# Kernel tuning notes

Hardware: AMD Instinct MI355X
Metric: run time of the kernel (lower is better)

Reference implementation:

```python
import jax, jax.numpy as jnp
import numpy as np

N_NODES = 50000
N_EDGES = 250000
D = 300
ATOM_VOCAB = 5001   # len(atom_map) + 1
WORD_VOCAB = 30000
N_GRAPHS = 1000
NUM_HOPS = 4


def setup_inputs() -> dict:
    key = jax.random.key(0)
    ks = jax.random.split(key, 6)
    x = jax.random.randint(ks[0], (N_NODES, 2), 0, 5000)            # (atom_id, word_id) per node
    edge_index = jax.random.randint(ks[1], (2, N_EDGES), 0, N_NODES)
    batch = jnp.sort(jax.random.randint(ks[2], (N_NODES,), 0, N_GRAPHS))
    atom_table = jax.random.normal(ks[3], (ATOM_VOCAB, D), dtype=jnp.float32) * 0.02
    word_table = jax.random.normal(ks[4], (WORD_VOCAB, D), dtype=jnp.float32) * 0.02
    W = jax.random.normal(ks[5], (D, D), dtype=jnp.float32) / jnp.sqrt(jnp.float32(D))
    b = jnp.zeros((D,), dtype=jnp.float32)
    return {"x": x, "edge_index": edge_index, "batch": batch, "num_hops": NUM_HOPS,
            "atom_table": atom_table, "word_table": word_table, "W": W, "b": b}


def reference(x, edge_index, batch, num_hops, atom_table, word_table, W, b):
    N = x.shape[0]
    # node embedding: atom + word lookup
    h = atom_table[x[:, 0]] + word_table[x[:, 1]]                    # [N, D]

    # GCN normalization with self-loops (PyG GCNConv defaults)
    loops = jnp.arange(N)
    src = jnp.concatenate([edge_index[0], loops])                    # [E+N]
    dst = jnp.concatenate([edge_index[1], loops])                    # [E+N]
    deg = jax.ops.segment_sum(jnp.ones_like(src, dtype=h.dtype), dst, num_segments=N)
    dinv = jax.lax.rsqrt(jnp.where(deg > 0, deg, 1.0))
    norm = dinv[src] * dinv[dst]                                     # [E+N]

    for _ in range(num_hops):
        hl = h @ W                                                   # [N, D] linear transform
        msg = hl[src] * norm[:, None]                                # gather + normalize
        h = jax.ops.segment_sum(msg, dst, num_segments=N) + b        # scatter-add + bias

    # global mean pool over graphs
    sums = jax.ops.segment_sum(h, batch, num_segments=N_GRAPHS)      # [G, D]
    counts = jax.ops.segment_sum(jnp.ones((N,), h.dtype), batch, num_segments=N_GRAPHS)
    return sums / jnp.clip(counts, 1.0)[:, None]
```

## Files before the change

### kernel.cpp

```cpp
#include <hip/hip_runtime.h>
#include <hip/hip_fp16.h>

#define D    300
#define DC   75
#define SCB  1024

typedef _Float16 half4v __attribute__((ext_vector_type(4)));

__global__ __launch_bounds__(256) void embed_f16(const int* __restrict__ x,
                                                 const float4* __restrict__ atomT,
                                                 const float4* __restrict__ wordT,
                                                 half4v* __restrict__ h, int N) {
    int idx = blockIdx.x * blockDim.x + threadIdx.x;
    if (idx >= N * DC) return;
    int n = idx / DC, c = idx - n * DC;
    int a = x[n * 2 + 0];
    int w = x[n * 2 + 1];
    float4 va = atomT[(size_t)a * DC + c];
    float4 vw = wordT[(size_t)w * DC + c];
    half4v o;
    o[0] = (_Float16)(va.x + vw.x);
    o[1] = (_Float16)(va.y + vw.y);
    o[2] = (_Float16)(va.z + vw.z);
    o[3] = (_Float16)(va.w + vw.w);
    h[idx] = o;
}

__global__ __launch_bounds__(256) void cnt_kernel(const int* __restrict__ dst, int* __restrict__ cnt, int E) {
    int i = blockIdx.x * blockDim.x + threadIdx.x;
    if (i < E) atomicAdd(&cnt[dst[i]], 1);
}

__global__ __launch_bounds__(SCB) void scan1_kernel(const int* __restrict__ cnt,
                                                    int* __restrict__ off, int* __restrict__ bsum,
                                                    float* __restrict__ dinv, int N) {
    __shared__ int warp_sums[16];
    const int tid = threadIdx.x;
    const int lane = tid & 63;
    const int wid = tid >> 6;
    int i = blockIdx.x * SCB + tid;
    int v = (i < N) ? cnt[i] : 0;
    if (i < N) dinv[i] = rsqrtf((float)(v + 1));
    int s = v;
    #pragma unroll
    for (int d = 1; d < 64; d <<= 1) {
        int t = __shfl_up(s, d, 64);
        if (lane >= d) s += t;
    }
    if (lane == 63) warp_sums[wid] = s;
    __syncthreads();
    if (wid == 0) {
        int ws = (lane < 16) ? warp_sums[lane] : 0;
        #pragma unroll
        for (int d = 1; d < 16; d <<= 1) {
            int t = __shfl_up(ws, d, 64);
            if (lane >= d) ws += t;
        }
        if (lane < 16) warp_sums[lane] = ws;
    }
    __syncthreads();
    int excl = (wid ? warp_sums[wid - 1] : 0) + s - v;
    if (i < N) off[i] = excl;
    if (tid == SCB - 1) bsum[blockIdx.x] = warp_sums[15];
}
__global__ __launch_bounds__(SCB) void scan2_kernel(int* __restrict__ bsum, int* __restrict__ bbase,
                                                    int* __restrict__ off, int nb, int N, int E) {
    __shared__ int warp_sums[16];
    const int tid = threadIdx.x;
    const int lane = tid & 63;
    const int wid = tid >> 6;
    int v = (tid < nb) ? bsum[tid] : 0;
    int s = v;
    #pragma unroll
    for (int d = 1; d < 64; d <<= 1) {
        int t = __shfl_up(s, d, 64);
        if (lane >= d) s += t;
    }
    if (lane == 63) warp_sums[wid] = s;
    __syncthreads();
    if (wid == 0) {
        int ws = (lane < 16) ? warp_sums[lane] : 0;
        #pragma unroll
        for (int d = 1; d < 16; d <<= 1) {
            int t = __shfl_up(ws, d, 64);
            if (lane >= d) ws += t;
        }
        if (lane < 16) warp_sums[lane] = ws;
    }
    __syncthreads();
    if (tid < nb) bbase[tid] = (wid ? warp_sums[wid - 1] : 0) + s - v;
    if (tid == 0) off[N] = E;
}
__global__ __launch_bounds__(256) void scan3_kernel(int* __restrict__ off, const int* __restrict__ bbase,
                                                    int* __restrict__ cursor, int N) {
    int i = blockIdx.x * blockDim.x + threadIdx.x;
    if (i >= N) return;
    int o = off[i] + bbase[i >> 10];
    off[i] = o;
    cursor[i] = o;
}

__global__ __launch_bounds__(256) void fill_kernel(const int* __restrict__ src, const int* __restrict__ dst,
                                                   const float* __restrict__ dinv, int* __restrict__ cursor,
                                                   int* __restrict__ csr_src, float* __restrict__ csr_w, int E) {
    int e = blockIdx.x * blockDim.x + threadIdx.x;
    if (e >= E) return;
    int s = src[e], d = dst[e];
    int slot = atomicAdd(&cursor[d], 1);
    csr_src[slot] = s;
    csr_w[slot] = dinv[s] * dinv[d];
}
__global__ __launch_bounds__(256) void seg_start_kernel(const int* __restrict__ batch,
                                                        int* __restrict__ start, int N, int G) {
    int i = blockIdx.x * blockDim.x + threadIdx.x;
    if (i >= N) return;
    int b = batch[i];
    int prev = (i == 0) ? -1 : batch[i - 1];
    for (int g = prev + 1; g <= b; ++g) start[g] = i;
    if (i == N - 1)
        for (int g = b + 1; g <= G; ++g) start[g] = N;
}

__global__ __launch_bounds__(256) void wprep1(const float* __restrict__ W, const float* __restrict__ bias,
                                              float* __restrict__ W2, float* __restrict__ w1b) {
    int bid = blockIdx.x;
    if (bid < 352) {
        int id = bid * 256 + threadIdx.x;
        if (id >= D * D) return;
        int i = id / D, j = id % D;
        float acc = 0.f;
        #pragma unroll 4
        for (int k = 0; k < D; ++k) acc = fmaf(W[i * D + k], W[k * D + j], acc);
        W2[id] = acc;
    } else {
        int j = threadIdx.x;
        if (j >= D) return;
        float acc = 0.f;
        #pragma unroll 4
        for (int k = 0; k < D; ++k) acc = fmaf(bias[k], W[k * D + j], acc);
        w1b[j] = acc;
    }
}
__global__ __launch_bounds__(256) void wprep2(const float* __restrict__ W2, const float* __restrict__ W,
                                              const float* __restrict__ w1b,
                                              float* __restrict__ W4, float* __restrict__ w2b,
                                              float* __restrict__ w3b) {
    int bid = blockIdx.x;
    if (bid < 352) {
        int id = bid * 256 + threadIdx.x;
        if (id >= D * D) return;
        int i = id / D, j = id % D;
        float acc = 0.f;
        #pragma unroll 4
        for (int k = 0; k < D; ++k) acc = fmaf(W2[i * D + k], W2[k * D + j], acc);
        W4[id] = acc;
    } else if (bid == 352) {
        int j = threadIdx.x;
        if (j >= D) return;
        float acc = 0.f;
        #pragma unroll 4
        for (int k = 0; k < D; ++k) acc = fmaf(w1b[k], W[k * D + j], acc);
        w2b[j] = acc;
    } else {
        int j = threadIdx.x;
        if (j >= D) return;
        float acc = 0.f;
        #pragma unroll 4
        for (int k = 0; k < D; ++k) acc = fmaf(w1b[k], W2[k * D + j], acc);
        w3b[j] = acc;
    }
}

__global__ __launch_bounds__(256) void gather_f16(const half4v* __restrict__ in,
                                                  const int* __restrict__ off,
                                                  const int* __restrict__ csr_src,
                                                  const float* __restrict__ csr_w,
                                                  const float* __restrict__ dinv,
                                                  const float* __restrict__ uin,
                                                  float* __restrict__ uout,
                                                  half4v* __restrict__ out, int N) {
    int idx = blockIdx.x * blockDim.x + threadIdx.x;
    if (idx >= N * DC) return;
    int n = idx / DC, c = idx - n * DC;
    float s = dinv[n]; s = s * s;
    half4v v0 = in[idx];
    float4 acc = make_float4(s * (float)v0[0], s * (float)v0[1], s * (float)v0[2], s * (float)v0[3]);
    const bool dou = (uout != nullptr) && (c == 0);
    float uacc = 0.f;
    if (dou) uacc = s * (uin ? uin[n] : 1.0f);
    int j0 = off[n], j1 = off[n + 1];
    for (int j = j0; j < j1; ++j) {
        int sn = csr_src[j];
        float w = csr_w[j];
        half4v u = in[(size_t)sn * DC + c];
        acc.x += w * (float)u[0]; acc.y += w * (float)u[1];
        acc.z += w * (float)u[2]; acc.w += w * (float)u[3];
        if (dou) uacc += w * (uin ? uin[sn] : 1.0f);
    }
    half4v o;
    o[0] = (_Float16)acc.x; o[1] = (_Float16)acc.y;
    o[2] = (_Float16)acc.z; o[3] = (_Float16)acc.w;
    out[idx] = o;
    if (dou) uout[n] = uacc;
}

__global__ __launch_bounds__(256) void pool_seg(const half4v* __restrict__ g4,
                                                const float* __restrict__ u1,
                                                const float* __restrict__ u2,
                                                const float* __restrict__ u3,
                                                const int* __restrict__ start,
                                                float* __restrict__ pg4, float* __restrict__ pu, int G) {
    int g = blockIdx.x;
    if (g >= G) return;
    int j0 = start[g], j1 = start[g + 1];
    float inv = (j1 > j0) ? 1.0f / (float)(j1 - j0) : 0.0f;
    int tid = threadIdx.x;
    if (tid < DC) {
        float4 acc = make_float4(0.f, 0.f, 0.f, 0.f);
        for (int n = j0; n < j1; ++n) {
            half4v v = g4[(size_t)n * DC + tid];
            acc.x += (float)v[0]; acc.y += (float)v[1];
            acc.z += (float)v[2]; acc.w += (float)v[3];
        }
        float4 o = make_float4(acc.x * inv, acc.y * inv, acc.z * inv, acc.w * inv);
        *(float4*)&pg4[(size_t)g * D + tid * 4] = o;
    } else if (tid == DC || tid == DC + 1 || tid == DC + 2) {
        const float* u = (tid == DC) ? u1 : (tid == DC + 1) ? u2 : u3;
        float acc = 0.f;
        for (int n = j0; n < j1; ++n) acc += u[n];
        pu[g * 4 + (tid - DC)] = acc * inv;
    } else if (tid == DC + 3) {
        pu[g * 4 + 3] = (j1 > j0) ? 1.0f : 0.0f;
    }
}

__global__ __launch_bounds__(256) void final_small(const float* __restrict__ pg4,
                                                   const float* __restrict__ pu,
                                                   const float* __restrict__ W4,
                                                   const float* __restrict__ w1b,
                                                   const float* __restrict__ w2b,
                                                   const float* __restrict__ w3b,
                                                   const float* __restrict__ bias,
                                                   float* __restrict__ out, int G) {
    __shared__ float row[D];
    int g = blockIdx.x;
    if (g >= G) return;
    int tid = threadIdx.x;
    for (int c = tid; c < D; c += 256) row[c] = pg4[(size_t)g * D + c];
    __syncthreads();
    float p1 = pu[g * 4 + 0], p2 = pu[g * 4 + 1], p3 = pu[g * 4 + 2], fl = pu[g * 4 + 3];
    for (int j = tid; j < D; j += 256) {
        float acc = 0.f;
        #pragma unroll 4
        for (int k = 0; k < D; ++k) acc = fmaf(row[k], W4[(size_t)k * D + j], acc);
        out[(size_t)g * D + j] = acc + p1 * w1b[j] + p2 * w2b[j] + p3 * w3b[j] + fl * bias[j];
    }
}

extern "C" void kernel_launch(void* const* d_in, const int* in_sizes, int n_in,
                              void* d_out, int out_size, void* d_ws, size_t ws_size,
                              hipStream_t stream) {
    (void)n_in; (void)ws_size;
    const int*   x     = (const int*)d_in[0];
    const int*   ei    = (const int*)d_in[1];
    const int*   batch = (const int*)d_in[2];
    const float* atomT = (const float*)d_in[4];
    const float* wordT = (const float*)d_in[5];
    const float* W     = (const float*)d_in[6];
    const float* bias  = (const float*)d_in[7];

    const int N = in_sizes[0] / 2;
    const int E = in_sizes[1] / 2;
    const int G = out_size / D;

    const int* src = ei;
    const int* dst = ei + E;

    _Float16* fA16   = (_Float16*)d_ws;
    _Float16* fB16   = fA16 + (size_t)N * D;
    float*    dinv   = (float*)(fB16 + (size_t)N * D);
    float*    csr_w  = dinv + N;
    float*    W2     = csr_w + E;
    float*    W4     = W2 + D * D;
    float*    w1b    = W4 + D * D;
    float*    w2b    = w1b + D;
    float*    w3b    = w2b + D;
    float*    u1     = w3b + D;
    float*    u2     = u1 + N;
    float*    u3     = u2 + N;
    float*    pg4    = u3 + N;
    float*    pu     = pg4 + (size_t)G * D;
    int*      cnt    = (int*)(pu + 4 * G);
    int*      off    = cnt + N;
    int*      cursor = off + N + 1;
    int*      csr_src= cursor + N;
    int*      bsum   = csr_src + E;
    int*      bbase  = bsum + 1024;
    int*      start  = bbase + 1024;

    const int B = 256;
    const int ndBlocks = (N * DC + B - 1) / B;
    const int nBlocks  = (N + B - 1) / B;
    const int nbScan   = (N + SCB - 1) / SCB;

    embed_f16<<<ndBlocks, B, 0, stream>>>(x, (const float4*)atomT, (const float4*)wordT, (half4v*)fA16, N);

    hipMemsetAsync(cnt, 0, (size_t)N * sizeof(int), stream);
    cnt_kernel<<<(E + B - 1) / B, B, 0, stream>>>(dst, cnt, E);
    scan1_kernel<<<nbScan, SCB, 0, stream>>>(cnt, off, bsum, dinv, N);
    scan2_kernel<<<1, SCB, 0, stream>>>(bsum, bbase, off, nbScan, N, E);
    scan3_kernel<<<nBlocks, B, 0, stream>>>(off, bbase, cursor, N);
    fill_kernel<<<(E + B - 1) / B, B, 0, stream>>>(src, dst, dinv, cursor, csr_src, csr_w, E);
    seg_start_kernel<<<nBlocks, B, 0, stream>>>(batch, start, N, G);

    wprep1<<<353, B, 0, stream>>>(W, bias, W2, w1b);
    wprep2<<<354, B, 0, stream>>>(W2, W, w1b, W4, w2b, w3b);

    gather_f16<<<ndBlocks, B, 0, stream>>>((const half4v*)fA16, off, csr_src, csr_w, dinv,
                                           nullptr, u1, (half4v*)fB16, N);
    gather_f16<<<ndBlocks, B, 0, stream>>>((const half4v*)fB16, off, csr_src, csr_w, dinv,
                                           u1, u2, (half4v*)fA16, N);
    gather_f16<<<ndBlocks, B, 0, stream>>>((const half4v*)fA16, off, csr_src, csr_w, dinv,
                                           u2, u3, (half4v*)fB16, N);
    gather_f16<<<ndBlocks, B, 0, stream>>>((const half4v*)fB16, off, csr_src, csr_w, dinv,
                                           nullptr, nullptr, (half4v*)fA16, N);

    pool_seg<<<G, B, 0, stream>>>((const half4v*)fA16, u1, u2, u3, start, pg4, pu, G);
    final_small<<<G, B, 0, stream>>>(pg4, pu, W4, w1b, w2b, w3b, bias, (float*)d_out, G);
}
```

Before: 384.2 us.

## Split node features into column panels for cache-local gathers with nontemporal CSR loads

Feature rows are now stored as 8 column panels of 10 half4 chunks each, padded from 75 to 80, and blocks are interleaved across panels. Each gather then touches a panel of about 4 MB instead of the full 30 MB feature matrix, so random neighbour reads are more likely to hit in L2/MALL. CSR index, weight loads and the output stores also use nontemporal hints so they do not evict feature data. The cost is padding waste of about 7%, CSR metadata being re-read once per panel, and changed indexing in the embed and pool kernels.

Result: slower. 574.2 us (+49.4%).

```diff
diff --git a/kernel.cpp b/kernel.cpp
--- a/kernel.cpp
+++ b/kernel.cpp
@@ -3,34 +3,40 @@
 
 #define D    300
 #define DC   75
+#define PNL  8
+#define PCH  10
 #define SCB  1024
 
 typedef _Float16 half4v __attribute__((ext_vector_type(4)));
 
-__global__ __launch_bounds__(256) void embed_f16(const int* __restrict__ x,
-                                                 const float4* __restrict__ atomT,
-                                                 const float4* __restrict__ wordT,
-                                                 half4v* __restrict__ h, int N) {
-    int idx = blockIdx.x * blockDim.x + threadIdx.x;
-    if (idx >= N * DC) return;
-    int n = idx / DC, c = idx - n * DC;
-    int a = x[n * 2 + 0];
-    int w = x[n * 2 + 1];
-    float4 va = atomT[(size_t)a * DC + c];
-    float4 vw = wordT[(size_t)w * DC + c];
-    half4v o;
-    o[0] = (_Float16)(va.x + vw.x);
-    o[1] = (_Float16)(va.y + vw.y);
-    o[2] = (_Float16)(va.z + vw.z);
-    o[3] = (_Float16)(va.w + vw.w);
-    h[idx] = o;
+__global__ __launch_bounds__(256) void embed_panel(const int* __restrict__ x,
+                                                   const float4* __restrict__ atomT,
+                                                   const float4* __restrict__ wordT,
+                                                   half4v* __restrict__ h, int N) {
+    int bid = blockIdx.x;
+    int p = bid & 7;
+    int chunk = (bid >> 3) * 256 + threadIdx.x;
+    if (chunk >= N * PCH) return;
+    int n = chunk / PCH, cc = chunk - n * PCH;
+    int c_lin = p * PCH + cc;
+    half4v o = (half4v)(_Float16)0;
+    if (c_lin < DC) {
+        int a = x[n * 2 + 0];
+        int w = x[n * 2 + 1];
+        float4 va = atomT[(size_t)a * DC + c_lin];
+        float4 vw = wordT[(size_t)w * DC + c_lin];
+        o[0] = (_Float16)(va.x + vw.x);
+        o[1] = (_Float16)(va.y + vw.y);
+        o[2] = (_Float16)(va.z + vw.z);
+        o[3] = (_Float16)(va.w + vw.w);
+    }
+    h[(size_t)p * N * PCH + chunk] = o;
 }
 
 __global__ __launch_bounds__(256) void cnt_kernel(const int* __restrict__ dst, int* __restrict__ cnt, int E) {
     int i = blockIdx.x * blockDim.x + threadIdx.x;
     if (i < E) atomicAdd(&cnt[dst[i]], 1);
 }
-
 __global__ __launch_bounds__(SCB) void scan1_kernel(const int* __restrict__ cnt,
                                                     int* __restrict__ off, int* __restrict__ bsum,
                                                     float* __restrict__ dinv, int N) {
@@ -99,7 +105,6 @@
     off[i] = o;
     cursor[i] = o;
 }
-
 __global__ __launch_bounds__(256) void fill_kernel(const int* __restrict__ src, const int* __restrict__ dst,
                                                    const float* __restrict__ dinv, int* __restrict__ cursor,
                                                    int* __restrict__ csr_src, float* __restrict__ csr_w, int E) {
@@ -171,28 +176,34 @@
     }
 }
 
-__global__ __launch_bounds__(256) void gather_f16(const half4v* __restrict__ in,
-                                                  const int* __restrict__ off,
-                                                  const int* __restrict__ csr_src,
-                                                  const float* __restrict__ csr_w,
-                                                  const float* __restrict__ dinv,
-                                                  const float* __restrict__ uin,
-                                                  float* __restrict__ uout,
-                                                  half4v* __restrict__ out, int N) {
-    int idx = blockIdx.x * blockDim.x + threadIdx.x;
-    if (idx >= N * DC) return;
-    int n = idx / DC, c = idx - n * DC;
+__global__ __launch_bounds__(256) void gather_panel(const half4v* __restrict__ in,
+                                                    const int* __restrict__ off,
+                                                    const int* __restrict__ csr_src,
+                                                    const float* __restrict__ csr_w,
+                                                    const float* __restrict__ dinv,
+                                                    const float* __restrict__ uin,
+                                                    float* __restrict__ uout,
+                                                    half4v* __restrict__ out, int N) {
+    int bid = blockIdx.x;
+    int p = bid & 7;
+    int chunk = (bid >> 3) * 256 + threadIdx.x;
+    if (chunk >= N * PCH) return;
+    int n = chunk / PCH, cc = chunk - n * PCH;
+    const half4v* pin = in + (size_t)p * N * PCH;
+
     float s = dinv[n]; s = s * s;
-    half4v v0 = in[idx];
+    half4v v0 = pin[chunk];
     float4 acc = make_float4(s * (float)v0[0], s * (float)v0[1], s * (float)v0[2], s * (float)v0[3]);
-    const bool dou = (uout != nullptr) && (c == 0);
+    const bool dou = (uout != nullptr) && (p == 0) && (cc == 0);
     float uacc = 0.f;
     if (dou) uacc = s * (uin ? uin[n] : 1.0f);
-    int j0 = off[n], j1 = off[n + 1];
+
+    int j0 = __builtin_nontemporal_load(&off[n]);
+    int j1 = __builtin_nontemporal_load(&off[n + 1]);
     for (int j = j0; j < j1; ++j) {
-        int sn = csr_src[j];
-        float w = csr_w[j];
-        half4v u = in[(size_t)sn * DC + c];
+        int sn = __builtin_nontemporal_load(&csr_src[j]);
+        float w = __builtin_nontemporal_load(&csr_w[j]);
+        half4v u = pin[(size_t)sn * PCH + cc];
         acc.x += w * (float)u[0]; acc.y += w * (float)u[1];
         acc.z += w * (float)u[2]; acc.w += w * (float)u[3];
         if (dou) uacc += w * (uin ? uin[sn] : 1.0f);
@@ -200,7 +211,7 @@
     half4v o;
     o[0] = (_Float16)acc.x; o[1] = (_Float16)acc.y;
     o[2] = (_Float16)acc.z; o[3] = (_Float16)acc.w;
-    out[idx] = o;
+    __builtin_nontemporal_store(o, &out[(size_t)p * N * PCH + chunk]);
     if (dou) uout[n] = uacc;
 }
 
@@ -209,27 +220,33 @@
                                                 const float* __restrict__ u2,
                                                 const float* __restrict__ u3,
                                                 const int* __restrict__ start,
-                                                float* __restrict__ pg4, float* __restrict__ pu, int G) {
+                                                float* __restrict__ pg4, float* __restrict__ pu,
+                                                int G, int N) {
     int g = blockIdx.x;
     if (g >= G) return;
     int j0 = start[g], j1 = start[g + 1];
     float inv = (j1 > j0) ? 1.0f / (float)(j1 - j0) : 0.0f;
     int tid = threadIdx.x;
-    if (tid < DC) {
-        float4 acc = make_float4(0.f, 0.f, 0.f, 0.f);
-        for (int n = j0; n < j1; ++n) {
-            half4v v = g4[(size_t)n * DC + tid];
-            acc.x += (float)v[0]; acc.y += (float)v[1];
-            acc.z += (float)v[2]; acc.w += (float)v[3];
+    if (tid < PNL * PCH) {
+        int p = tid / PCH, cc = tid - p * PCH;
+        int c_lin = p * PCH + cc;
+        if (c_lin < DC) {
+            const half4v* pg = g4 + (size_t)p * N * PCH;
+            float4 acc = make_float4(0.f, 0.f, 0.f, 0.f);
+            for (int n = j0; n < j1; ++n) {
+                half4v v = pg[(size_t)n * PCH + cc];
+                acc.x += (float)v[0]; acc.y += (float)v[1];
+                acc.z += (float)v[2]; acc.w += (float)v[3];
+            }
+            float4 o = make_float4(acc.x * inv, acc.y * inv, acc.z * inv, acc.w * inv);
+            *(float4*)&pg4[(size_t)g * D + c_lin * 4] = o;
         }
-        float4 o = make_float4(acc.x * inv, acc.y * inv, acc.z * inv, acc.w * inv);
-        *(float4*)&pg4[(size_t)g * D + tid * 4] = o;
-    } else if (tid == DC || tid == DC + 1 || tid == DC + 2) {
-        const float* u = (tid == DC) ? u1 : (tid == DC + 1) ? u2 : u3;
+    } else if (tid >= 80 && tid <= 82) {
+        const float* u = (tid == 80) ? u1 : (tid == 81) ? u2 : u3;
         float acc = 0.f;
         for (int n = j0; n < j1; ++n) acc += u[n];
-        pu[g * 4 + (tid - DC)] = acc * inv;
-    } else if (tid == DC + 3) {
+        pu[g * 4 + (tid - 80)] = acc * inv;
+    } else if (tid == 83) {
         pu[g * 4 + 3] = (j1 > j0) ? 1.0f : 0.0f;
     }
 }
@@ -277,8 +294,8 @@
     const int* dst = ei + E;
 
     _Float16* fA16   = (_Float16*)d_ws;
-    _Float16* fB16   = fA16 + (size_t)N * D;
-    float*    dinv   = (float*)(fB16 + (size_t)N * D);
+    _Float16* fB16   = fA16 + (size_t)PNL * N * PCH * 4;
+    float*    dinv   = (float*)(fB16 + (size_t)PNL * N * PCH * 4);
     float*    csr_w  = dinv + N;
     float*    W2     = csr_w + E;
     float*    W4     = W2 + D * D;
@@ -299,11 +316,13 @@
     int*      start  = bbase + 1024;
 
     const int B = 256;
-    const int ndBlocks = (N * DC + B - 1) / B;
     const int nBlocks  = (N + B - 1) / B;
     const int nbScan   = (N + SCB - 1) / SCB;
-
-    embed_f16<<<ndBlocks, B, 0, stream>>>(x, (const float4*)atomT, (const float4*)wordT, (half4v*)fA16, N);
+    const int nbPanel  = (N * PCH + B - 1) / B;
+    const int panelGrid = nbPanel * PNL;
+
+    embed_panel<<<panelGrid, B, 0, stream>>>(x, (const float4*)atomT, (const float4*)wordT,
+                                             (half4v*)fA16, N);
 
     hipMemsetAsync(cnt, 0, (size_t)N * sizeof(int), stream);
     cnt_kernel<<<(E + B - 1) / B, B, 0, stream>>>(dst, cnt, E);
@@ -316,15 +335,15 @@
     wprep1<<<353, B, 0, stream>>>(W, bias, W2, w1b);
     wprep2<<<354, B, 0, stream>>>(W2, W, w1b, W4, w2b, w3b);
 
-    gather_f16<<<ndBlocks, B, 0, stream>>>((const half4v*)fA16, off, csr_src, csr_w, dinv,
-                                           nullptr, u1, (half4v*)fB16, N);
-    gather_f16<<<ndBlocks, B, 0, stream>>>((const half4v*)fB16, off, csr_src, csr_w, dinv,
-                                           u1, u2, (half4v*)fA16, N);
-    gather_f16<<<ndBlocks, B, 0, stream>>>((const half4v*)fA16, off, csr_src, csr_w, dinv,
-                                           u2, u3, (half4v*)fB16, N);
-    gather_f16<<<ndBlocks, B, 0, stream>>>((const half4v*)fB16, off, csr_src, csr_w, dinv,
-                                           nullptr, nullptr, (half4v*)fA16, N);
-
-    pool_seg<<<G, B, 0, stream>>>((const half4v*)fA16, u1, u2, u3, start, pg4, pu, G);
+    gather_panel<<<panelGrid, B, 0, stream>>>((const half4v*)fA16, off, csr_src, csr_w, dinv,
+                                              nullptr, u1, (half4v*)fB16, N);
+    gather_panel<<<panelGrid, B, 0, stream>>>((const half4v*)fB16, off, csr_src, csr_w, dinv,
+                                              u1, u2, (half4v*)fA16, N);
+    gather_panel<<<panelGrid, B, 0, stream>>>((const half4v*)fA16, off, csr_src, csr_w, dinv,
+                                              u2, u3, (half4v*)fB16, N);
+    gather_panel<<<panelGrid, B, 0, stream>>>((const half4v*)fB16, off, csr_src, csr_w, dinv,
+                                              nullptr, nullptr, (half4v*)fA16, N);
+
+    pool_seg<<<G, B, 0, stream>>>((const half4v*)fA16, u1, u2, u3, start, pg4, pu, G, N);
     final_small<<<G, B, 0, stream>>>(pg4, pu, W4, w1b, w2b, w3b, bias, (float*)d_out, G);
 }
```
